# Performance work log

Measured on AMD Instinct MI355X. Metric: run time of the kernel, lower is better.

Reference implementation:

```python
import jax, jax.numpy as jnp
import numpy as np

N = 4096     # num nodes
FEAT = 500   # knn attribute dim
HID = 512    # args.hid_dim
E = 65536    # edges (avg degree 16)
T = 8        # args.time -> euler steps with step_size=1


def setup_inputs() -> dict:
    key = jax.random.key(0)
    ks = jax.random.split(key, 10)
    knn = jax.random.normal(ks[0], (N, FEAT), jnp.float32)
    adj = jax.random.uniform(ks[1], (N, N), jnp.float32)
    norm_factor = jnp.ones((), jnp.float32)
    edge_index = jax.random.randint(ks[2], (2, E), 0, N, dtype=jnp.int32).astype(jnp.int64)
    edge_weight = jax.random.uniform(ks[3], (E,), jnp.float32)
    # AGCN params (init eye + small noise so math is non-trivial)
    w1 = jnp.eye(N, dtype=jnp.float32) + 0.01 * jax.random.normal(ks[4], (N, N), jnp.float32)
    w2 = jnp.eye(N, dtype=jnp.float32) + 0.01 * jax.random.normal(ks[5], (N, N), jnp.float32)
    # extractor: Linear(N, HID) then Linear(HID, HID), kaiming-normal (relu), zero bias
    W0 = jax.random.normal(ks[6], (HID, N), jnp.float32) * np.float32((2.0 / N) ** 0.5)
    b0 = jnp.zeros((HID,), jnp.float32)
    W1 = jax.random.normal(ks[7], (HID, HID), jnp.float32) * np.float32((2.0 / HID) ** 0.5)
    b1 = jnp.zeros((HID,), jnp.float32)
    # LaplacianODEFunc scalar params
    alpha_train = jnp.asarray(0.5, jnp.float32)
    beta_train = jnp.asarray(0.1, jnp.float32)
    return dict(knn=knn, adj=adj, norm_factor=norm_factor, w1=w1, w2=w2,
                W0=W0, b0=b0, W1=W1, b1=b1, edge_weight=edge_weight,
                alpha_train=alpha_train, beta_train=beta_train, edge_index=edge_index)


def _spmm(edge_index, edge_weight, x):
    # out[row] += w * x[col], row=edge_index[0], col=edge_index[1]
    msg = edge_weight[:, None] * x[edge_index[1]]          # [E, HID]
    return jax.ops.segment_sum(msg, edge_index[0], num_segments=x.shape[0])


def reference(knn, adj, norm_factor, w1, w2, W0, b0, W1, b1,
              edge_weight, alpha_train, beta_train, edge_index):
    # ---- AGCN ----
    H = (adj @ w1) @ adj.T                                  # [N, N]
    H = (H @ w2) @ knn                                      # [N, FEAT]
    embed = H @ H.T                                         # [N, N]
    norm = jnp.maximum(jnp.linalg.norm(embed, axis=1, keepdims=True), 1e-12)
    embed = embed / norm                                    # F.normalize(dim=1)
    # ---- extractor MLP (no activation in source; dropout=eval no-op) ----
    h = embed @ W0.T + b0                                   # [N, HID]
    h = h @ W1.T + b1                                       # [N, HID]
    # ---- ODE diffusion: dx/dt = sigmoid(a)*(Ax - x) + b*x0, explicit Euler dt=1 ----
    x0 = jax.lax.stop_gradient(h)
    alpha = jax.nn.sigmoid(alpha_train)

    def step(x, _):
        ax = _spmm(edge_index, edge_weight, x)
        return x + alpha * (ax - x) + beta_train * x0, None

    z_ode, _ = jax.lax.scan(step, h, None, length=T)
    z = jax.nn.relu(norm_factor * z_ode + h)
    z = (z - z.mean(0)) / jnp.std(z, ddof=1)                # torch std is unbiased
    return z
```

## Files before the change

kernel.cpp:

```cpp
#include <hip/hip_runtime.h>
#include <stdint.h>
#include <stddef.h>

typedef __bf16 bf16;
typedef __attribute__((ext_vector_type(8))) __bf16 bf16x8;
typedef __attribute__((ext_vector_type(4))) __bf16 bf16x4;
typedef __attribute__((ext_vector_type(4))) float f32x4;

#define NN 4096
#define HIDD 512
#define NE 65536

__device__ inline void gll16(const void* g, void* l) {
    __builtin_amdgcn_global_load_lds(
        (const __attribute__((address_space(1))) void*)g,
        (__attribute__((address_space(3))) void*)l, 16, 0, 0);
}

__global__ void cvt_f32_bf16(const float* __restrict__ in, bf16* __restrict__ out, int n) {
    int i = (blockIdx.x * 256 + threadIdx.x) * 4;
    if (i >= n) return;
    float4 v = *reinterpret_cast<const float4*>(in + i);
    bf16x4 o;
    o[0] = (bf16)v.x; o[1] = (bf16)v.y; o[2] = (bf16)v.z; o[3] = (bf16)v.w;
    *reinterpret_cast<bf16x4*>(out + i) = o;
}

__global__ void reduce_slices_bf16(const float* __restrict__ in, bf16* __restrict__ out,
                                   int n, int S) {
    int i = (blockIdx.x * 256 + threadIdx.x) * 4;
    if (i >= n) return;
    float4 s = make_float4(0.f, 0.f, 0.f, 0.f);
    for (int k = 0; k < S; ++k) {
        float4 v = *reinterpret_cast<const float4*>(in + (size_t)k * n + i);
        s.x += v.x; s.y += v.y; s.z += v.z; s.w += v.w;
    }
    bf16x4 o;
    o[0] = (bf16)s.x; o[1] = (bf16)s.y; o[2] = (bf16)s.z; o[3] = (bf16)s.w;
    *reinterpret_cast<bf16x4*>(out + i) = o;
}

__global__ void transpose_pad_f32(const float* __restrict__ in, bf16* __restrict__ out,
                                  int R, int C, int Cpad) {
    __shared__ bf16 tile[32][33];
    int c0 = blockIdx.x * 32, r0 = blockIdx.y * 32;
    int tx = threadIdx.x, ty = threadIdx.y;
    for (int i = ty; i < 32; i += 8) {
        int r = r0 + i, c = c0 + tx;
        bf16 v = (bf16)0.f;
        if (r < R && c < C) v = (bf16)in[(size_t)r * C + c];
        tile[i][tx] = v;
    }
    __syncthreads();
    for (int i = ty; i < 32; i += 8) {
        int oc = c0 + i, orow = r0 + tx;
        if (oc < Cpad && orow < R) out[(size_t)oc * R + orow] = tile[tx][i];
    }
}

__global__ void transpose_bf16(const bf16* __restrict__ in, bf16* __restrict__ out,
                               int R, int C) {
    __shared__ bf16 tile[32][33];
    int c0 = blockIdx.x * 32, r0 = blockIdx.y * 32;
    int tx = threadIdx.x, ty = threadIdx.y;
    for (int i = ty; i < 32; i += 8)
        tile[i][tx] = in[(size_t)(r0 + i) * C + c0 + tx];
    __syncthreads();
    for (int i = ty; i < 32; i += 8)
        out[(size_t)(c0 + i) * R + r0 + tx] = tile[tx][i];
}

template<bool BF16_OUT, bool HAS_BIAS, bool ROW_SCALE>
__global__ __launch_bounds__(256)
void gemm_nt(const bf16* __restrict__ A, const bf16* __restrict__ B,
             void* __restrict__ Cp, const float* __restrict__ bias,
             const float* __restrict__ rowscale, int M, int N, int K) {
    __shared__ __align__(16) bf16 As[128 * 32];
    __shared__ __align__(16) bf16 Bs[128 * 32];
    const int tid  = threadIdx.x;
    const int wave = tid >> 6;
    const int lane = tid & 63;
    const int m0 = blockIdx.y * 128, n0 = blockIdx.x * 128;
    const int lrow = lane >> 2;
    const int lcol = (lane & 3) * 8;
    const int c0 = wave * 2;
    const size_t arow0 = (size_t)(m0 + c0 * 16 + lrow) * K + lcol;
    const size_t arow1 = (size_t)(m0 + (c0 + 1) * 16 + lrow) * K + lcol;
    const size_t brow0 = (size_t)(n0 + c0 * 16 + lrow) * K + lcol;
    const size_t brow1 = (size_t)(n0 + (c0 + 1) * 16 + lrow) * K + lcol;
    bf16* asd0 = &As[c0 * 512];
    bf16* asd1 = &As[(c0 + 1) * 512];
    bf16* bsd0 = &Bs[c0 * 512];
    bf16* bsd1 = &Bs[(c0 + 1) * 512];

    f32x4 acc[4][4] = {};

    const int wm = (wave >> 1) * 64;
    const int wn = (wave & 1) * 64;
    const int fm = wm + (lane & 15);
    const int fn = wn + (lane & 15);
    const int fk = (lane >> 4) * 8;

    const int kper = K / gridDim.z;
    const int kz0 = blockIdx.z * kper;
    const int kz1 = kz0 + kper;

    for (int k0 = kz0; k0 < kz1; k0 += 32) {
        gll16(A + arow0 + k0, asd0);
        gll16(A + arow1 + k0, asd1);
        gll16(B + brow0 + k0, bsd0);
        gll16(B + brow1 + k0, bsd1);
        __syncthreads();
        bf16x8 af[4], bg[4];
#pragma unroll
        for (int i = 0; i < 4; ++i)
            af[i] = *reinterpret_cast<const bf16x8*>(&As[(fm + i * 16) * 32 + fk]);
#pragma unroll
        for (int j = 0; j < 4; ++j)
            bg[j] = *reinterpret_cast<const bf16x8*>(&Bs[(fn + j * 16) * 32 + fk]);
#pragma unroll
        for (int i = 0; i < 4; ++i)
#pragma unroll
            for (int j = 0; j < 4; ++j)
                acc[i][j] = __builtin_amdgcn_mfma_f32_16x16x32_bf16(af[i], bg[j], acc[i][j], 0, 0, 0);
        __syncthreads();
    }

    const int rbase = m0 + wm + (lane >> 4) * 4;
    const int cbase = n0 + wn + (lane & 15);
    bf16*  outb = (bf16*)Cp;
    float* outf = (float*)Cp + (size_t)blockIdx.z * M * N;
#pragma unroll
    for (int i = 0; i < 4; ++i) {
#pragma unroll
        for (int j = 0; j < 4; ++j) {
            int col = cbase + j * 16;
            float bv = 0.f;
            if (HAS_BIAS) bv = bias[col];
#pragma unroll
            for (int r = 0; r < 4; ++r) {
                int row = rbase + i * 16 + r;
                float v = acc[i][j][r];
                if (ROW_SCALE) v *= rowscale[row];
                v += bv;
                if (BF16_OUT) outb[(size_t)row * N + col] = (bf16)v;
                else          outf[(size_t)row * N + col] = v;
            }
        }
    }
}

__global__ void colnorm(const bf16* __restrict__ Ht, const float* __restrict__ Rf,
                        float* __restrict__ inv) {
    int i = blockIdx.x * 256 + threadIdx.x;
    float s = 0.f;
    for (int a = 0; a < HIDD; ++a)
        s += Rf[(size_t)a * NN + i] * (float)Ht[(size_t)a * NN + i];
    inv[i] = 1.f / fmaxf(sqrtf(s), 1e-12f);
}

__global__ void csr_count(const int* __restrict__ ei, int* __restrict__ cnt, int E) {
    int e = blockIdx.x * 256 + threadIdx.x;
    if (e < E) atomicAdd(&cnt[ei[e]], 1);
}

__global__ void scan_4096(const int* __restrict__ cnt, int* __restrict__ rs) {
    __shared__ int s[1024];
    int t = threadIdx.x;
    int b = t * 4;
    int a0 = cnt[b], a1 = cnt[b + 1], a2 = cnt[b + 2], a3 = cnt[b + 3];
    int tot = a0 + a1 + a2 + a3;
    s[t] = tot;
    __syncthreads();
    for (int off = 1; off < 1024; off <<= 1) {
        int v = (t >= off) ? s[t - off] : 0;
        __syncthreads();
        s[t] += v;
        __syncthreads();
    }
    int excl = s[t] - tot;
    rs[b] = excl; rs[b + 1] = excl + a0; rs[b + 2] = excl + a0 + a1; rs[b + 3] = excl + a0 + a1 + a2;
    if (t == 1023) rs[4096] = s[1023];
}

__global__ void csr_scatter(const int* __restrict__ ei, const float* __restrict__ ew,
                            int* __restrict__ cur, int* __restrict__ ccol,
                            float* __restrict__ cw, int E) {
    int e = blockIdx.x * 256 + threadIdx.x;
    if (e < E) {
        int r = ei[e];
        int p = atomicAdd(&cur[r], 1);
        ccol[p] = ei[E + e];
        cw[p] = ew[e];
    }
}

__global__ void ode_step(const float* __restrict__ xin, const float* __restrict__ x0,
                         float* __restrict__ xout, const int* __restrict__ rs,
                         const int* __restrict__ ccol, const float* __restrict__ cw,
                         const float* __restrict__ alpha_p, const float* __restrict__ beta_p) {
    int row = blockIdx.x, t = threadIdx.x;
    float alpha = 1.f / (1.f + expf(-alpha_p[0]));
    float beta = beta_p[0];
    const float4* xin4 = (const float4*)xin;
    float4 acc = make_float4(0.f, 0.f, 0.f, 0.f);
    int p0 = rs[row], p1 = rs[row + 1];
    for (int p = p0; p < p1; ++p) {
        int c = ccol[p]; float w = cw[p];
        float4 v = xin4[(size_t)c * 128 + t];
        acc.x += w * v.x; acc.y += w * v.y; acc.z += w * v.z; acc.w += w * v.w;
    }
    float4 xi = xin4[(size_t)row * 128 + t];
    float4 xz = ((const float4*)x0)[(size_t)row * 128 + t];
    float4 r;
    r.x = xi.x + alpha * (acc.x - xi.x) + beta * xz.x;
    r.y = xi.y + alpha * (acc.y - xi.y) + beta * xz.y;
    r.z = xi.z + alpha * (acc.z - xi.z) + beta * xz.z;
    r.w = xi.w + alpha * (acc.w - xi.w) + beta * xz.w;
    ((float4*)xout)[(size_t)row * 128 + t] = r;
}

__global__ void epi1(const float* __restrict__ x8, const float* __restrict__ h,
                     const float* __restrict__ nf_p, float* __restrict__ z,
                     float* __restrict__ colsum, float* __restrict__ gst) {
    __shared__ float r1[512], r2[512];
    int b = blockIdx.x, j = threadIdx.x;
    float nf = nf_p[0];
    float cp = 0.f, sq = 0.f;
    for (int i = 0; i < 8; ++i) {
        size_t idx = (size_t)(b * 8 + i) * HIDD + j;
        float v = nf * x8[idx] + h[idx];
        v = fmaxf(v, 0.f);
        z[idx] = v;
        cp += v; sq += v * v;
    }
    atomicAdd(&colsum[j], cp);
    r1[j] = cp; r2[j] = sq;
    __syncthreads();
    for (int off = 256; off > 0; off >>= 1) {
        if (j < off) { r1[j] += r1[j + off]; r2[j] += r2[j + off]; }
        __syncthreads();
    }
    if (j == 0) { atomicAdd(&gst[0], r1[0]); atomicAdd(&gst[1], r2[0]); }
}

__global__ void epi2(const float* __restrict__ z, const float* __restrict__ colsum,
                     const float* __restrict__ gst, float* __restrict__ out) {
    size_t idx = (size_t)blockIdx.x * 256 + threadIdx.x;
    int j = (int)(idx & (HIDD - 1));
    float n = (float)NN * (float)HIDD;
    float gmean = gst[0] / n;
    float var = (gst[1] - n * gmean * gmean) / (n - 1.f);
    float istd = rsqrtf(var);
    float mean = colsum[j] * (1.f / (float)NN);
    out[idx] = (z[idx] - mean) * istd;
}

extern "C" void kernel_launch(void* const* d_in, const int* in_sizes, int n_in,
                              void* d_out, int out_size, void* d_ws, size_t ws_size,
                              hipStream_t stream) {
    const float* knn  = (const float*)d_in[0];
    const float* adj  = (const float*)d_in[1];
    const float* nf   = (const float*)d_in[2];
    const float* w1   = (const float*)d_in[3];
    const float* w2   = (const float*)d_in[4];
    const float* W0   = (const float*)d_in[5];
    const float* b0   = (const float*)d_in[6];
    const float* W1   = (const float*)d_in[7];
    const float* b1   = (const float*)d_in[8];
    const float* ew   = (const float*)d_in[9];
    const float* alph = (const float*)d_in[10];
    const float* beta = (const float*)d_in[11];
    const int*   ei   = (const int*)d_in[12];

    char* w = (char*)d_ws;
    size_t off = 0;
    auto alloc = [&](size_t bytes) -> char* {
        char* p = w + off;
        off += (bytes + 255) & ~(size_t)255;
        return p;
    };
    const size_t SZ_NN  = (size_t)NN * NN * sizeof(bf16);
    const size_t SZ_TH  = (size_t)HIDD * NN * sizeof(bf16);
    bf16* Bar  = (bf16*)alloc(SZ_NN);
    bf16* Car  = (bf16*)alloc(SZ_NN);
    bf16* knnT = (bf16*)alloc(SZ_TH);
    bf16* tA   = (bf16*)alloc(SZ_TH);
    bf16* tB   = (bf16*)alloc(SZ_TH);
    float* tf  = (float*)alloc((size_t)16 * 1024 * 1024);
    bf16* Hm   = (bf16*)alloc(SZ_TH);
    bf16* Gb   = (bf16*)alloc((size_t)HIDD * HIDD * sizeof(bf16));
    bf16* M0tb = (bf16*)alloc((size_t)HIDD * HIDD * sizeof(bf16));
    bf16* h1b  = (bf16*)alloc((size_t)NN * HIDD * sizeof(bf16));
    float* hf  = (float*)alloc((size_t)NN * HIDD * sizeof(float));
    float* inv = (float*)alloc(NN * sizeof(float));
    int*  cnt  = (int*)alloc(NN * sizeof(int));
    int*  rs   = (int*)alloc((NN + 1) * sizeof(int));
    int*  cur  = (int*)alloc(NN * sizeof(int));
    int*  ccol = (int*)alloc(NE * sizeof(int));
    float* cw  = (float*)alloc(NE * sizeof(float));
    float* colsum = (float*)alloc(HIDD * sizeof(float));
    float* gst = (float*)alloc(2 * sizeof(float));
    float* xA = (float*)Car;
    float* xB = (float*)Car + (size_t)NN * HIDD;
    (void)ws_size; (void)n_in; (void)in_sizes; (void)out_size;

    dim3 tb(32, 8);
    const int nTH = HIDD * NN;
    const int nHH = HIDD * HIDD;

    transpose_pad_f32<<<dim3(16, 128), tb, 0, stream>>>(knn, knnT, NN, 500, HIDD);
    cvt_f32_bf16<<<(NN * NN) / 1024, 256, 0, stream>>>(w2, Car, NN * NN);
    transpose_pad_f32<<<dim3(128, 128), tb, 0, stream>>>(adj, Bar, NN, NN, NN);

    gemm_nt<false, false, false><<<dim3(32, 4, 2), 256, 0, stream>>>(knnT, Car, tf, nullptr, nullptr, HIDD, NN, NN);
    reduce_slices_bf16<<<nTH / 1024, 256, 0, stream>>>(tf, tA, nTH, 2);
    gemm_nt<false, false, false><<<dim3(32, 4, 2), 256, 0, stream>>>(tA, Bar, tf, nullptr, nullptr, HIDD, NN, NN);
    reduce_slices_bf16<<<nTH / 1024, 256, 0, stream>>>(tf, tB, nTH, 2);
    cvt_f32_bf16<<<(NN * NN) / 1024, 256, 0, stream>>>(w1, Car, NN * NN);
    gemm_nt<false, false, false><<<dim3(32, 4, 2), 256, 0, stream>>>(tB, Car, tf, nullptr, nullptr, HIDD, NN, NN);
    reduce_slices_bf16<<<nTH / 1024, 256, 0, stream>>>(tf, tA, nTH, 2);
    cvt_f32_bf16<<<(NN * NN) / 1024, 256, 0, stream>>>(adj, Bar, NN * NN);
    gemm_nt<false, false, false><<<dim3(32, 4, 2), 256, 0, stream>>>(tA, Bar, tf, nullptr, nullptr, HIDD, NN, NN);
    reduce_slices_bf16<<<nTH / 1024, 256, 0, stream>>>(tf, tB, nTH, 2);

    transpose_bf16<<<dim3(128, 16), tb, 0, stream>>>(tB, Hm, HIDD, NN);

    gemm_nt<false, false, false><<<dim3(4, 4, 8), 256, 0, stream>>>(tB, tB, tf, nullptr, nullptr, HIDD, HIDD, NN);
    reduce_slices_bf16<<<nHH / 1024, 256, 0, stream>>>(tf, Gb, nHH, 8);

    gemm_nt<false, false, false><<<dim3(32, 4, 1), 256, 0, stream>>>(Gb, Hm, tf, nullptr, nullptr, HIDD, NN, HIDD);
    colnorm<<<NN / 256, 256, 0, stream>>>(tB, tf, inv);

    cvt_f32_bf16<<<(HIDD * NN) / 1024, 256, 0, stream>>>(W0, Car, HIDD * NN);
    gemm_nt<false, false, false><<<dim3(4, 4, 8), 256, 0, stream>>>(Car, tB, tf, nullptr, nullptr, HIDD, HIDD, NN);
    reduce_slices_bf16<<<nHH / 1024, 256, 0, stream>>>(tf, M0tb, nHH, 8);

    gemm_nt<true, true, true><<<dim3(4, 32, 1), 256, 0, stream>>>(Hm, M0tb, h1b, b0, inv, NN, HIDD, HIDD);
    cvt_f32_bf16<<<(HIDD * HIDD) / 1024, 256, 0, stream>>>(W1, (bf16*)((char*)Car + 16 * 1024 * 1024), HIDD * HIDD);
    bf16* W1b = (bf16*)((char*)Car + 16 * 1024 * 1024);
    gemm_nt<false, true, false><<<dim3(4, 32, 1), 256, 0, stream>>>(h1b, W1b, hf, b1, nullptr, NN, HIDD, HIDD);

    hipMemsetAsync(cnt, 0, NN * sizeof(int), stream);
    csr_count<<<NE / 256, 256, 0, stream>>>(ei, cnt, NE);
    scan_4096<<<1, 1024, 0, stream>>>(cnt, rs);
    hipMemcpyAsync(cur, rs, NN * sizeof(int), hipMemcpyDeviceToDevice, stream);
    csr_scatter<<<NE / 256, 256, 0, stream>>>(ei, ew, cur, ccol, cw, NE);

    const float* xi = hf;
    float* xo = xA;
    for (int s = 0; s < 8; ++s) {
        ode_step<<<NN, 128, 0, stream>>>(xi, hf, xo, rs, ccol, cw, alph, beta);
        xi = xo;
        xo = (s % 2 == 0) ? xB : xA;
    }

    hipMemsetAsync(colsum, 0, HIDD * sizeof(float), stream);
    hipMemsetAsync(gst, 0, 2 * sizeof(float), stream);
    epi1<<<NN / 8, 512, 0, stream>>>(xB, hf, nf, tf, colsum, gst);
    epi2<<<(NN * HIDD) / 256, 256, 0, stream>>>(tf, colsum, gst, (float*)d_out);
}
```

Measured before the change: 778.0 us.

## Use bf16 split-K partials with more slices, bf16 ODE state, and split colnorm

Split-K GEMM partial outputs are now written as bf16 instead of fp32, and the split factor is doubled (2→4 for the big N×N products, 8→16 for the K=4096 HIDD×HIDD products), with a new 8-wide bf16 reduction kernel. The MLP output and the ODE iteration state are stored in bf16, and the ODE step maps one 64-lane wave per row. The column-norm reduction is split across blocks with atomics plus a finalize kernel. The aim is to cut memory traffic and raise parallelism, at the cost of extra rounding error from bf16 partial sums and from bf16 ODE state accumulated across eight steps.

```diff
diff --git a/kernel.cpp b/kernel.cpp
--- a/kernel.cpp
+++ b/kernel.cpp
@@ -26,18 +26,20 @@
     *reinterpret_cast<bf16x4*>(out + i) = o;
 }
 
-__global__ void reduce_slices_bf16(const float* __restrict__ in, bf16* __restrict__ out,
+__global__ void reduce_bf16_slices(const bf16* __restrict__ in, bf16* __restrict__ out,
                                    int n, int S) {
-    int i = (blockIdx.x * 256 + threadIdx.x) * 4;
+    int i = (blockIdx.x * 256 + threadIdx.x) * 8;
     if (i >= n) return;
-    float4 s = make_float4(0.f, 0.f, 0.f, 0.f);
+    float acc[8] = {};
     for (int k = 0; k < S; ++k) {
-        float4 v = *reinterpret_cast<const float4*>(in + (size_t)k * n + i);
-        s.x += v.x; s.y += v.y; s.z += v.z; s.w += v.w;
-    }
-    bf16x4 o;
-    o[0] = (bf16)s.x; o[1] = (bf16)s.y; o[2] = (bf16)s.z; o[3] = (bf16)s.w;
-    *reinterpret_cast<bf16x4*>(out + i) = o;
+        bf16x8 v = *reinterpret_cast<const bf16x8*>(in + (size_t)k * n + i);
+#pragma unroll
+        for (int j = 0; j < 8; ++j) acc[j] += (float)v[j];
+    }
+    bf16x8 o;
+#pragma unroll
+    for (int j = 0; j < 8; ++j) o[j] = (bf16)acc[j];
+    *reinterpret_cast<bf16x8*>(out + i) = o;
 }
 
 __global__ void transpose_pad_f32(const float* __restrict__ in, bf16* __restrict__ out,
@@ -70,7 +72,7 @@
         out[(size_t)(c0 + i) * R + r0 + tx] = tile[tx][i];
 }
 
-template<bool BF16_OUT, bool HAS_BIAS, bool ROW_SCALE>
+template<int OMODE, bool HAS_BIAS, bool ROW_SCALE>
 __global__ __launch_bounds__(256)
 void gemm_nt(const bf16* __restrict__ A, const bf16* __restrict__ B,
              void* __restrict__ Cp, const float* __restrict__ bias,
@@ -128,8 +130,9 @@
 
     const int rbase = m0 + wm + (lane >> 4) * 4;
     const int cbase = n0 + wn + (lane & 15);
+    float* outf = (float*)Cp + (size_t)blockIdx.z * M * N;
     bf16*  outb = (bf16*)Cp;
-    float* outf = (float*)Cp + (size_t)blockIdx.z * M * N;
+    bf16*  outp = (bf16*)Cp + (size_t)blockIdx.z * M * N;
 #pragma unroll
     for (int i = 0; i < 4; ++i) {
 #pragma unroll
@@ -143,20 +146,27 @@
                 float v = acc[i][j][r];
                 if (ROW_SCALE) v *= rowscale[row];
                 v += bv;
-                if (BF16_OUT) outb[(size_t)row * N + col] = (bf16)v;
-                else          outf[(size_t)row * N + col] = v;
+                if (OMODE == 0)      outf[(size_t)row * N + col] = v;
+                else if (OMODE == 1) outb[(size_t)row * N + col] = (bf16)v;
+                else                 outp[(size_t)row * N + col] = (bf16)v;
             }
         }
     }
 }
 
-__global__ void colnorm(const bf16* __restrict__ Ht, const float* __restrict__ Rf,
-                        float* __restrict__ inv) {
+__global__ void colnorm_part(const bf16* __restrict__ Ht, const float* __restrict__ Rf,
+                             float* __restrict__ n2) {
+    int i = blockIdx.x * 128 + threadIdx.x;
+    int a0 = blockIdx.y * 64;
+    float s = 0.f;
+    for (int a = a0; a < a0 + 64; ++a)
+        s += Rf[(size_t)a * NN + i] * (float)Ht[(size_t)a * NN + i];
+    atomicAdd(&n2[i], s);
+}
+
+__global__ void colnorm_fin(const float* __restrict__ n2, float* __restrict__ inv) {
     int i = blockIdx.x * 256 + threadIdx.x;
-    float s = 0.f;
-    for (int a = 0; a < HIDD; ++a)
-        s += Rf[(size_t)a * NN + i] * (float)Ht[(size_t)a * NN + i];
-    inv[i] = 1.f / fmaxf(sqrtf(s), 1e-12f);
+    inv[i] = 1.f / fmaxf(sqrtf(n2[i]), 1e-12f);
 }
 
 __global__ void csr_count(const int* __restrict__ ei, int* __restrict__ cnt, int E) {
@@ -195,32 +205,35 @@
     }
 }
 
-__global__ void ode_step(const float* __restrict__ xin, const float* __restrict__ x0,
-                         float* __restrict__ xout, const int* __restrict__ rs,
-                         const int* __restrict__ ccol, const float* __restrict__ cw,
-                         const float* __restrict__ alpha_p, const float* __restrict__ beta_p) {
-    int row = blockIdx.x, t = threadIdx.x;
+__global__ void ode_step_bf16(const bf16* __restrict__ xin, const bf16* __restrict__ x0,
+                              bf16* __restrict__ xout, const int* __restrict__ rs,
+                              const int* __restrict__ ccol, const float* __restrict__ cw,
+                              const float* __restrict__ alpha_p, const float* __restrict__ beta_p) {
+    int row = blockIdx.x * 4 + (threadIdx.x >> 6);
+    int lane = threadIdx.x & 63;
     float alpha = 1.f / (1.f + expf(-alpha_p[0]));
     float beta = beta_p[0];
-    const float4* xin4 = (const float4*)xin;
-    float4 acc = make_float4(0.f, 0.f, 0.f, 0.f);
+    const bf16x8* xin8 = (const bf16x8*)xin;
+    float acc[8] = {};
     int p0 = rs[row], p1 = rs[row + 1];
     for (int p = p0; p < p1; ++p) {
         int c = ccol[p]; float w = cw[p];
-        float4 v = xin4[(size_t)c * 128 + t];
-        acc.x += w * v.x; acc.y += w * v.y; acc.z += w * v.z; acc.w += w * v.w;
-    }
-    float4 xi = xin4[(size_t)row * 128 + t];
-    float4 xz = ((const float4*)x0)[(size_t)row * 128 + t];
-    float4 r;
-    r.x = xi.x + alpha * (acc.x - xi.x) + beta * xz.x;
-    r.y = xi.y + alpha * (acc.y - xi.y) + beta * xz.y;
-    r.z = xi.z + alpha * (acc.z - xi.z) + beta * xz.z;
-    r.w = xi.w + alpha * (acc.w - xi.w) + beta * xz.w;
-    ((float4*)xout)[(size_t)row * 128 + t] = r;
-}
-
-__global__ void epi1(const float* __restrict__ x8, const float* __restrict__ h,
+        bf16x8 v = xin8[(size_t)c * 64 + lane];
+#pragma unroll
+        for (int j = 0; j < 8; ++j) acc[j] += w * (float)v[j];
+    }
+    bf16x8 xi = xin8[(size_t)row * 64 + lane];
+    bf16x8 xz = ((const bf16x8*)x0)[(size_t)row * 64 + lane];
+    bf16x8 r;
+#pragma unroll
+    for (int j = 0; j < 8; ++j) {
+        float x = (float)xi[j];
+        r[j] = (bf16)(x + alpha * (acc[j] - x) + beta * (float)xz[j]);
+    }
+    ((bf16x8*)xout)[(size_t)row * 64 + lane] = r;
+}
+
+__global__ void epi1(const bf16* __restrict__ x8, const bf16* __restrict__ h,
                      const float* __restrict__ nf_p, float* __restrict__ z,
                      float* __restrict__ colsum, float* __restrict__ gst) {
     __shared__ float r1[512], r2[512];
@@ -229,7 +242,7 @@
     float cp = 0.f, sq = 0.f;
     for (int i = 0; i < 8; ++i) {
         size_t idx = (size_t)(b * 8 + i) * HIDD + j;
-        float v = nf * x8[idx] + h[idx];
+        float v = nf * (float)x8[idx] + (float)h[idx];
         v = fmaxf(v, 0.f);
         z[idx] = v;
         cp += v; sq += v * v;
@@ -292,8 +305,9 @@
     bf16* Gb   = (bf16*)alloc((size_t)HIDD * HIDD * sizeof(bf16));
     bf16* M0tb = (bf16*)alloc((size_t)HIDD * HIDD * sizeof(bf16));
     bf16* h1b  = (bf16*)alloc((size_t)NN * HIDD * sizeof(bf16));
-    float* hf  = (float*)alloc((size_t)NN * HIDD * sizeof(float));
+    bf16* hb   = (bf16*)alloc((size_t)NN * HIDD * sizeof(bf16));
     float* inv = (float*)alloc(NN * sizeof(float));
+    float* n2  = (float*)alloc(NN * sizeof(float));
     int*  cnt  = (int*)alloc(NN * sizeof(int));
     int*  rs   = (int*)alloc((NN + 1) * sizeof(int));
     int*  cur  = (int*)alloc(NN * sizeof(int));
@@ -301,8 +315,10 @@
     float* cw  = (float*)alloc(NE * sizeof(float));
     float* colsum = (float*)alloc(HIDD * sizeof(float));
     float* gst = (float*)alloc(2 * sizeof(float));
-    float* xA = (float*)Car;
-    float* xB = (float*)Car + (size_t)NN * HIDD;
+    bf16* tfb = (bf16*)tf;
+    bf16* W1b = (bf16*)((char*)Car + 16 * 1024 * 1024);
+    bf16* xA  = (bf16*)Car;
+    bf16* xB  = (bf16*)Car + (size_t)NN * HIDD;
     (void)ws_size; (void)n_in; (void)in_sizes; (void)out_size;
 
     dim3 tb(32, 8);
@@ -313,33 +329,34 @@
     cvt_f32_bf16<<<(NN * NN) / 1024, 256, 0, stream>>>(w2, Car, NN * NN);
     transpose_pad_f32<<<dim3(128, 128), tb, 0, stream>>>(adj, Bar, NN, NN, NN);
 
-    gemm_nt<false, false, false><<<dim3(32, 4, 2), 256, 0, stream>>>(knnT, Car, tf, nullptr, nullptr, HIDD, NN, NN);
-    reduce_slices_bf16<<<nTH / 1024, 256, 0, stream>>>(tf, tA, nTH, 2);
-    gemm_nt<false, false, false><<<dim3(32, 4, 2), 256, 0, stream>>>(tA, Bar, tf, nullptr, nullptr, HIDD, NN, NN);
-    reduce_slices_bf16<<<nTH / 1024, 256, 0, stream>>>(tf, tB, nTH, 2);
+    gemm_nt<2, false, false><<<dim3(32, 4, 4), 256, 0, stream>>>(knnT, Car, tfb, nullptr, nullptr, HIDD, NN, NN);
+    reduce_bf16_slices<<<nTH / 2048, 256, 0, stream>>>(tfb, tA, nTH, 4);
+    gemm_nt<2, false, false><<<dim3(32, 4, 4), 256, 0, stream>>>(tA, Bar, tfb, nullptr, nullptr, HIDD, NN, NN);
+    reduce_bf16_slices<<<nTH / 2048, 256, 0, stream>>>(tfb, tB, nTH, 4);
     cvt_f32_bf16<<<(NN * NN) / 1024, 256, 0, stream>>>(w1, Car, NN * NN);
-    gemm_nt<false, false, false><<<dim3(32, 4, 2), 256, 0, stream>>>(tB, Car, tf, nullptr, nullptr, HIDD, NN, NN);
-    reduce_slices_bf16<<<nTH / 1024, 256, 0, stream>>>(tf, tA, nTH, 2);
+    gemm_nt<2, false, false><<<dim3(32, 4, 4), 256, 0, stream>>>(tB, Car, tfb, nullptr, nullptr, HIDD, NN, NN);
+    reduce_bf16_slices<<<nTH / 2048, 256, 0, stream>>>(tfb, tA, nTH, 4);
     cvt_f32_bf16<<<(NN * NN) / 1024, 256, 0, stream>>>(adj, Bar, NN * NN);
-    gemm_nt<false, false, false><<<dim3(32, 4, 2), 256, 0, stream>>>(tA, Bar, tf, nullptr, nullptr, HIDD, NN, NN);
-    reduce_slices_bf16<<<nTH / 1024, 256, 0, stream>>>(tf, tB, nTH, 2);
+    gemm_nt<2, false, false><<<dim3(32, 4, 4), 256, 0, stream>>>(tA, Bar, tfb, nullptr, nullptr, HIDD, NN, NN);
+    reduce_bf16_slices<<<nTH / 2048, 256, 0, stream>>>(tfb, tB, nTH, 4);
 
     transpose_bf16<<<dim3(128, 16), tb, 0, stream>>>(tB, Hm, HIDD, NN);
 
-    gemm_nt<false, false, false><<<dim3(4, 4, 8), 256, 0, stream>>>(tB, tB, tf, nullptr, nullptr, HIDD, HIDD, NN);
-    reduce_slices_bf16<<<nHH / 1024, 256, 0, stream>>>(tf, Gb, nHH, 8);
-
-    gemm_nt<false, false, false><<<dim3(32, 4, 1), 256, 0, stream>>>(Gb, Hm, tf, nullptr, nullptr, HIDD, NN, HIDD);
-    colnorm<<<NN / 256, 256, 0, stream>>>(tB, tf, inv);
+    gemm_nt<2, false, false><<<dim3(4, 4, 16), 256, 0, stream>>>(tB, tB, tfb, nullptr, nullptr, HIDD, HIDD, NN);
+    reduce_bf16_slices<<<nHH / 2048, 256, 0, stream>>>(tfb, Gb, nHH, 16);
+
+    gemm_nt<0, false, false><<<dim3(32, 4, 1), 256, 0, stream>>>(Gb, Hm, tf, nullptr, nullptr, HIDD, NN, HIDD);
+    hipMemsetAsync(n2, 0, NN * sizeof(float), stream);
+    colnorm_part<<<dim3(32, 8), 128, 0, stream>>>(tB, tf, n2);
+    colnorm_fin<<<NN / 256, 256, 0, stream>>>(n2, inv);
 
     cvt_f32_bf16<<<(HIDD * NN) / 1024, 256, 0, stream>>>(W0, Car, HIDD * NN);
-    gemm_nt<false, false, false><<<dim3(4, 4, 8), 256, 0, stream>>>(Car, tB, tf, nullptr, nullptr, HIDD, HIDD, NN);
-    reduce_slices_bf16<<<nHH / 1024, 256, 0, stream>>>(tf, M0tb, nHH, 8);
-
-    gemm_nt<true, true, true><<<dim3(4, 32, 1), 256, 0, stream>>>(Hm, M0tb, h1b, b0, inv, NN, HIDD, HIDD);
-    cvt_f32_bf16<<<(HIDD * HIDD) / 1024, 256, 0, stream>>>(W1, (bf16*)((char*)Car + 16 * 1024 * 1024), HIDD * HIDD);
-    bf16* W1b = (bf16*)((char*)Car + 16 * 1024 * 1024);
-    gemm_nt<false, true, false><<<dim3(4, 32, 1), 256, 0, stream>>>(h1b, W1b, hf, b1, nullptr, NN, HIDD, HIDD);
+    gemm_nt<2, false, false><<<dim3(4, 4, 16), 256, 0, stream>>>(Car, tB, tfb, nullptr, nullptr, HIDD, HIDD, NN);
+    reduce_bf16_slices<<<nHH / 2048, 256, 0, stream>>>(tfb, M0tb, nHH, 16);
+
+    gemm_nt<1, true, true><<<dim3(4, 32, 1), 256, 0, stream>>>(Hm, M0tb, h1b, b0, inv, NN, HIDD, HIDD);
+    cvt_f32_bf16<<<(HIDD * HIDD) / 1024, 256, 0, stream>>>(W1, W1b, HIDD * HIDD);
+    gemm_nt<1, true, false><<<dim3(4, 32, 1), 256, 0, stream>>>(h1b, W1b, hb, b1, nullptr, NN, HIDD, HIDD);
 
     hipMemsetAsync(cnt, 0, NN * sizeof(int), stream);
     csr_count<<<NE / 256, 256, 0, stream>>>(ei, cnt, NE);
@@ -347,16 +364,16 @@
     hipMemcpyAsync(cur, rs, NN * sizeof(int), hipMemcpyDeviceToDevice, stream);
     csr_scatter<<<NE / 256, 256, 0, stream>>>(ei, ew, cur, ccol, cw, NE);
 
-    const float* xi = hf;
-    float* xo = xA;
+    const bf16* xi = hb;
+    bf16* xo = xA;
     for (int s = 0; s < 8; ++s) {
-        ode_step<<<NN, 128, 0, stream>>>(xi, hf, xo, rs, ccol, cw, alph, beta);
+        ode_step_bf16<<<NN / 4, 256, 0, stream>>>(xi, hb, xo, rs, ccol, cw, alph, beta);
         xi = xo;
         xo = (s % 2 == 0) ? xB : xA;
     }
 
     hipMemsetAsync(colsum, 0, HIDD * sizeof(float), stream);
     hipMemsetAsync(gst, 0, 2 * sizeof(float), stream);
-    epi1<<<NN / 8, 512, 0, stream>>>(xB, hf, nf, tf, colsum, gst);
+    epi1<<<NN / 8, 512, 0, stream>>>(xB, hb, nf, tf, colsum, gst);
     epi2<<<(NN * HIDD) / 256, 256, 0, stream>>>(tf, colsum, gst, (float*)d_out);
 }
```

Measured after the change: 675.5 us. 1.15x faster.
